# Kernel tuning notes

Measured on AMD Instinct MI355X. Metric: run time of the kernel, lower is better.

## Reference

```python
import jax, jax.numpy as jnp
import numpy as np

TOKENS, D_MODEL, D_FF, RANK = 16384, 1024, 2816, 16


def setup_inputs() -> dict:
    key = jax.random.key(0)
    ks = jax.random.split(key, 7)
    s = lambda k, shp, scale: jax.random.normal(k, shp, dtype=jnp.float32) * scale
    return {
        "x": s(ks[0], (TOKENS, D_MODEL), 1.0),
        "W_gate_up": s(ks[1], (D_MODEL, 2 * D_FF), 0.02),
        "A_gate_up": s(ks[2], (D_MODEL, RANK), 0.02),
        "B_gate_up": s(ks[3], (RANK, 2 * D_FF), 0.02),
        "W_down": s(ks[4], (D_FF, D_MODEL), 0.02),
        "A_down": s(ks[5], (D_FF, RANK), 0.02),
        "B_down": s(ks[6], (RANK, D_MODEL), 0.02),
    }


def reference(x, W_gate_up, A_gate_up, B_gate_up, W_down, A_down, B_down):
    # gate_up_proj: base GEMM + LoRA low-rank correction
    gate_up = x @ W_gate_up + (x @ A_gate_up) @ B_gate_up  # [T, 2*D_FF]
    gate, up = jnp.split(gate_up, 2, axis=-1)
    h = jax.nn.silu(gate) * up  # SiluAndMul, [T, D_FF]
    # down_proj: base GEMM + LoRA correction
    out = h @ W_down + (h @ A_down) @ B_down  # [T, D_MODEL]
    return out
```

## Files before the change

### kernel.cpp

```cpp
#include <hip/hip_runtime.h>


typedef __bf16 bf16_t;
typedef __bf16 bf16x4 __attribute__((ext_vector_type(4)));
typedef __bf16 bf16x8 __attribute__((ext_vector_type(8)));
typedef float f32x4 __attribute__((ext_vector_type(4)));

#define TOKENS 16384
#define DMODEL 1024
#define DFF    2816
#define N2F    5632

#define BARM() asm volatile("s_barrier" ::: "memory")
#define VMW(n) asm volatile("s_waitcnt vmcnt(" #n ")" ::: "memory")
#define MFMA(d, va, vb) d = __builtin_amdgcn_mfma_f32_16x16x32_bf16(va, vb, d, 0, 0, 0)
#define LD8(p) (*(const bf16x8*)(p))
#define SGB(m, n) __builtin_amdgcn_sched_group_barrier(m, n, 0)
#define SGB_PATTERN2() do {                                                       \
    SGB(0x010, 8);                                                                \
    SGB(0x100, 2); SGB(0x008, 5);                                                 \
    SGB(0x100, 2); SGB(0x008, 5);                                                 \
    SGB(0x100, 2); SGB(0x008, 5);                                                 \
    SGB(0x100, 2); SGB(0x008, 5);                                                 \
    SGB(0x100, 2); SGB(0x008, 5);                                                 \
    SGB(0x100, 2); SGB(0x008, 5);                                                 \
    SGB(0x100, 2); SGB(0x008, 5);                                                 \
    SGB(0x100, 2); SGB(0x008, 5);                                                 \
    SGB(0x100, 2); SGB(0x008, 5);                                                 \
    SGB(0x100, 2); SGB(0x008, 5);                                                 \
    SGB(0x100, 2); SGB(0x008, 7);                                                 \
    SGB(0x100, 2); SGB(0x008, 7); } while (0)

__device__ __forceinline__ void gload16(const bf16_t* g, bf16_t* l) {
    __builtin_amdgcn_global_load_lds(
        (const __attribute__((address_space(1))) void*)g,
        (__attribute__((address_space(3))) void*)l, 16, 0, 0);
}

template<int KTOT, int NTOT>
__global__ __launch_bounds__(256) void prep_weff(
        const float* __restrict__ W, const float* __restrict__ A,
        const float* __restrict__ B, bf16_t* __restrict__ Wt) {
    __shared__ float Ws[64][65];
    __shared__ float As[64][17];
    __shared__ float Bs[16][64];
    const int t = threadIdx.x;
    const int k0 = blockIdx.x * 64, n0 = blockIdx.y * 64;
    #pragma unroll
    for (int i = 0; i < 16; ++i) {
        int row = i * 4 + t / 64, col = t % 64;
        Ws[row][col] = W[(size_t)(k0 + row) * NTOT + n0 + col];
    }
    #pragma unroll
    for (int i = 0; i < 4; ++i) {
        int idx = i * 256 + t;
        As[idx / 16][idx % 16] = A[(size_t)(k0 + idx / 16) * 16 + idx % 16];
    }
    #pragma unroll
    for (int i = 0; i < 4; ++i) {
        int idx = i * 256 + t;
        Bs[idx / 64][idx % 64] = B[(size_t)(idx / 64) * NTOT + n0 + idx % 64];
    }
    __syncthreads();
    const int kl = t % 64;
    #pragma unroll
    for (int j = 0; j < 16; ++j) {
        int nl = j * 4 + t / 64;
        float val = Ws[kl][nl];
        #pragma unroll
        for (int r = 0; r < 16; ++r) val += As[kl][r] * Bs[r][nl];
        Wt[(size_t)(n0 + nl) * KTOT + k0 + kl] = (bf16_t)val;
    }
}

__global__ __launch_bounds__(256) void conv_bf16(
        const float* __restrict__ in, bf16_t* __restrict__ out, int n4) {
    int i = blockIdx.x * 256 + threadIdx.x;
    if (i < n4) {
        float4 v = ((const float4*)in)[i];
        bf16x4 o;
        o.x = (bf16_t)v.x; o.y = (bf16_t)v.y; o.z = (bf16_t)v.z; o.w = (bf16_t)v.w;
        ((bf16x4*)out)[i] = o;
    }
}

__global__ __launch_bounds__(512, 2) void gemm1(
        const bf16_t* __restrict__ X, const bf16_t* __restrict__ Wt,
        bf16_t* __restrict__ H) {
    __shared__ bf16_t lds[65536];
    const int t = threadIdx.x, l = t & 63;
    const int wid = t >> 6, wr = wid >> 2, wc = wid & 3;
    const int l15 = l & 15, lhi = l >> 4;
    const int wgl = ((int)blockIdx.x & 7) * 176 + ((int)blockIdx.x >> 3);
    const int tf = wgl % 22, tm = wgl / 22;
    const int mbase = tm * 256, fbase = tf * 128;
    const int srow = t >> 2;
    const int sc8 = ((t & 3) ^ (srow & 3)) * 8;
    const bf16_t* gA  = X + (size_t)(mbase + srow) * DMODEL + sc8;
    const bf16_t* gA2 = gA + (size_t)128 * DMODEL;
    const bf16_t* gBg = Wt + (size_t)(fbase + srow) * DMODEL + sc8;
    const bf16_t* gBu = Wt + (size_t)(DFF + fbase + srow) * DMODEL + sc8;
    const int rsw = (lhi ^ (l15 & 3)) * 8;
    const int aoff = (wr * 128 + l15) * 32 + rsw;
    const int boff = 8192 + (wc * 32 + l15) * 32 + rsw;

    f32x4 accg[8][2] = {}, accu[8][2] = {};
    bf16x8 a0[8], g0[2], u0[2], a1[8], g1[2], u1[2];
    const int NT1 = DMODEL / 32;

#define G1_STAGE(kt) do { const int kc = (kt) * 32;                               \
    bf16_t* p = lds + (((kt) & 3) << 14) + wid * 512;                             \
    gload16(gA  + kc, p);                                                         \
    gload16(gA2 + kc, p + 4096);                                                  \
    gload16(gBg + kc, p + 8192);                                                  \
    gload16(gBu + kc, p + 12288); } while (0)
#define G1_READ(aa, gg, uu, bi) do {                                              \
    const bf16_t* _pa = lds + ((bi) << 14) + aoff;                                \
    aa[0] = LD8(_pa);        aa[1] = LD8(_pa + 512);                              \
    aa[2] = LD8(_pa + 1024); aa[3] = LD8(_pa + 1536);                             \
    aa[4] = LD8(_pa + 2048); aa[5] = LD8(_pa + 2560);                             \
    aa[6] = LD8(_pa + 3072); aa[7] = LD8(_pa + 3584);                             \
    const bf16_t* _pb = lds + ((bi) << 14) + boff;                                \
    gg[0] = LD8(_pb);        gg[1] = LD8(_pb + 512);                              \
    uu[0] = LD8(_pb + 4096); uu[1] = LD8(_pb + 4608); } while (0)
#define G1_MFMA(aa, gg, uu) do {                                                  \
    _Pragma("unroll")                                                             \
    for (int m = 0; m < 8; ++m) {                                                 \
        MFMA(accg[m][0], aa[m], gg[0]); MFMA(accu[m][0], aa[m], uu[0]);           \
        MFMA(accg[m][1], aa[m], gg[1]); MFMA(accu[m][1], aa[m], uu[1]);           \
    } } while (0)

    G1_STAGE(0); G1_STAGE(1);
    VMW(0); BARM();
    G1_STAGE(2); G1_STAGE(3);
    G1_READ(a0, g0, u0, 0);
    G1_READ(a1, g1, u1, 1);
    G1_MFMA(a0, g0, u0);
    for (int s2 = 2; s2 <= NT1 - 2; s2 += 2) {
        VMW(0); BARM();
        if (s2 + 2 < NT1) { G1_STAGE(s2 + 2); G1_STAGE(s2 + 3); }
        G1_READ(a0, g0, u0, s2 & 3);
        G1_MFMA(a1, g1, u1);
        G1_READ(a1, g1, u1, (s2 + 1) & 3);
        G1_MFMA(a0, g0, u0);
        SGB_PATTERN2();
    }
    G1_MFMA(a1, g1, u1);
#undef G1_STAGE
#undef G1_READ
#undef G1_MFMA

    #pragma unroll
    for (int m = 0; m < 8; ++m)
        #pragma unroll
        for (int n = 0; n < 2; ++n)
            #pragma unroll
            for (int r = 0; r < 4; ++r) {
                int row = mbase + wr * 128 + m * 16 + lhi * 4 + r;
                int col = fbase + wc * 32 + n * 16 + l15;
                float g = accg[m][n][r], u = accu[m][n][r];
                H[(size_t)row * DFF + col] = (bf16_t)(g / (1.0f + __expf(-g)) * u);
            }
}

__global__ __launch_bounds__(512, 2) void gemm2(
        const bf16_t* __restrict__ Hm, const bf16_t* __restrict__ Wt,
        float* __restrict__ O) {
    __shared__ bf16_t lds[65536];
    const int t = threadIdx.x, l = t & 63;
    const int wid = t >> 6, wr = wid >> 2, wc = wid & 3;
    const int l15 = l & 15, lhi = l >> 4;
    const int wgl = ((int)blockIdx.x & 7) * 32 + ((int)blockIdx.x >> 3);
    const int tn = wgl % 4, tm = wgl / 4;
    const int mbase = tm * 256, nbase = tn * 256;
    const int srow = t >> 2;
    const int sc8 = ((t & 3) ^ (srow & 3)) * 8;
    const bf16_t* gA  = Hm + (size_t)(mbase + srow) * DFF + sc8;
    const bf16_t* gA2 = gA + (size_t)128 * DFF;
    const bf16_t* gB  = Wt + (size_t)(nbase + srow) * DFF + sc8;
    const bf16_t* gB2 = gB + (size_t)128 * DFF;
    const int rsw = (lhi ^ (l15 & 3)) * 8;
    const int aoff = (wr * 128 + l15) * 32 + rsw;
    const int boff = 8192 + (wc * 64 + l15) * 32 + rsw;

    f32x4 acc[8][4] = {};
    bf16x8 a0[8], b0[4], a1[8], b1[4];
    const int NT2 = DFF / 32;

#define G2_STAGE(kt) do { const int kc = (kt) * 32;                               \
    bf16_t* p = lds + (((kt) & 3) << 14) + wid * 512;                             \
    gload16(gA  + kc, p);                                                         \
    gload16(gA2 + kc, p + 4096);                                                  \
    gload16(gB  + kc, p + 8192);                                                  \
    gload16(gB2 + kc, p + 12288); } while (0)
#define G2_READ(aa, bb, bi) do {                                                  \
    const bf16_t* _pa = lds + ((bi) << 14) + aoff;                                \
    aa[0] = LD8(_pa);        aa[1] = LD8(_pa + 512);                              \
    aa[2] = LD8(_pa + 1024); aa[3] = LD8(_pa + 1536);                             \
    aa[4] = LD8(_pa + 2048); aa[5] = LD8(_pa + 2560);                             \
    aa[6] = LD8(_pa + 3072); aa[7] = LD8(_pa + 3584);                             \
    const bf16_t* _pb = lds + ((bi) << 14) + boff;                                \
    bb[0] = LD8(_pb);        bb[1] = LD8(_pb + 512);                              \
    bb[2] = LD8(_pb + 1024); bb[3] = LD8(_pb + 1536); } while (0)
#define G2_MFMA(aa, bb) do {                                                      \
    _Pragma("unroll")                                                             \
    for (int m = 0; m < 8; ++m) {                                                 \
        MFMA(acc[m][0], aa[m], bb[0]); MFMA(acc[m][1], aa[m], bb[1]);             \
        MFMA(acc[m][2], aa[m], bb[2]); MFMA(acc[m][3], aa[m], bb[3]);             \
    } } while (0)

    G2_STAGE(0); G2_STAGE(1);
    VMW(0); BARM();
    G2_STAGE(2); G2_STAGE(3);
    G2_READ(a0, b0, 0);
    G2_READ(a1, b1, 1);
    G2_MFMA(a0, b0);
    for (int s2 = 2; s2 <= NT2 - 2; s2 += 2) {
        VMW(0); BARM();
        if (s2 + 2 < NT2) { G2_STAGE(s2 + 2); G2_STAGE(s2 + 3); }
        G2_READ(a0, b0, s2 & 3);
        G2_MFMA(a1, b1);
        G2_READ(a1, b1, (s2 + 1) & 3);
        G2_MFMA(a0, b0);
        SGB_PATTERN2();
    }
    G2_MFMA(a1, b1);
#undef G2_STAGE
#undef G2_READ
#undef G2_MFMA

    #pragma unroll
    for (int m = 0; m < 8; ++m)
        #pragma unroll
        for (int n = 0; n < 4; ++n)
            #pragma unroll
            for (int r = 0; r < 4; ++r) {
                int row = mbase + wr * 128 + m * 16 + lhi * 4 + r;
                int col = nbase + wc * 64 + n * 16 + l15;
                O[(size_t)row * DMODEL + col] = acc[m][n][r];
            }
}

extern "C" void kernel_launch(void* const* d_in, const int* in_sizes, int n_in,
                              void* d_out, int out_size, void* d_ws, size_t ws_size,
                              hipStream_t stream) {
    const float* x   = (const float*)d_in[0];
    const float* Wgu = (const float*)d_in[1];
    const float* Agu = (const float*)d_in[2];
    const float* Bgu = (const float*)d_in[3];
    const float* Wd  = (const float*)d_in[4];
    const float* Ad  = (const float*)d_in[5];
    const float* Bd  = (const float*)d_in[6];
    float* out = (float*)d_out;
    char* ws = (char*)d_ws;

    bf16_t* wgut = (bf16_t*)(ws);
    bf16_t* wdt  = (bf16_t*)(ws + 11534336);
    bf16_t* xb   = (bf16_t*)(ws + 17301504);
    bf16_t* hb   = (bf16_t*)(ws + 50855936);

    prep_weff<DMODEL, N2F><<<dim3(DMODEL / 64, N2F / 64), 256, 0, stream>>>(
        Wgu, Agu, Bgu, wgut);
    prep_weff<DFF, DMODEL><<<dim3(DFF / 64, DMODEL / 64), 256, 0, stream>>>(
        Wd, Ad, Bd, wdt);
    conv_bf16<<<(TOKENS * DMODEL / 4) / 256, 256, 0, stream>>>(
        x, xb, TOKENS * DMODEL / 4);
    gemm1<<<22 * 64, 512, 0, stream>>>(xb, wgut, hb);
    gemm2<<<8 * 32, 512, 0, stream>>>(hb, wdt, out);
}
```

Baseline: 327.6 us.

## Restructure gemm1 K-loop into per-tile pipeline with 3-deep prefetch and partial waits

```diff
diff --git a/kernel.cpp b/kernel.cpp
--- a/kernel.cpp
+++ b/kernel.cpp
@@ -16,6 +16,14 @@
 #define MFMA(d, va, vb) d = __builtin_amdgcn_mfma_f32_16x16x32_bf16(va, vb, d, 0, 0, 0)
 #define LD8(p) (*(const bf16x8*)(p))
 #define SGB(m, n) __builtin_amdgcn_sched_group_barrier(m, n, 0)
+#define SGB_PATTERN() do {                                                        \
+    SGB(0x010, 4);                                                                \
+    SGB(0x100, 2); SGB(0x008, 5);                                                 \
+    SGB(0x100, 2); SGB(0x008, 5);                                                 \
+    SGB(0x100, 2); SGB(0x008, 5);                                                 \
+    SGB(0x100, 2); SGB(0x008, 5);                                                 \
+    SGB(0x100, 2); SGB(0x008, 6);                                                 \
+    SGB(0x100, 2); SGB(0x008, 6); } while (0)
 #define SGB_PATTERN2() do {                                                       \
     SGB(0x010, 8);                                                                \
     SGB(0x100, 2); SGB(0x008, 5);                                                 \
@@ -129,23 +137,25 @@
         MFMA(accg[m][0], aa[m], gg[0]); MFMA(accu[m][0], aa[m], uu[0]);           \
         MFMA(accg[m][1], aa[m], gg[1]); MFMA(accu[m][1], aa[m], uu[1]);           \
     } } while (0)
-
-    G1_STAGE(0); G1_STAGE(1);
+#define G1_ITER(kt, aaU, ggU, uuU, aaR, ggR, uuR) do {                            \
+    VMW(4); BARM();                                                               \
+    if ((kt) + 3 < NT1) G1_STAGE((kt) + 3);                                       \
+    G1_READ(aaR, ggR, uuR, ((kt) + 1) & 3);                                       \
+    G1_MFMA(aaU, ggU, uuU);                                                       \
+    SGB_PATTERN(); } while (0)
+
+    G1_STAGE(0); G1_STAGE(1); G1_STAGE(2);
+    VMW(8); BARM();
+    G1_READ(a0, g0, u0, 0);
+    for (int kt2 = 0; kt2 < NT1 - 2; kt2 += 2) {
+        G1_ITER(kt2,     a0, g0, u0, a1, g1, u1);
+        G1_ITER(kt2 + 1, a1, g1, u1, a0, g0, u0);
+    }
     VMW(0); BARM();
-    G1_STAGE(2); G1_STAGE(3);
-    G1_READ(a0, g0, u0, 0);
-    G1_READ(a1, g1, u1, 1);
+    G1_READ(a1, g1, u1, (NT1 - 1) & 3);
     G1_MFMA(a0, g0, u0);
-    for (int s2 = 2; s2 <= NT1 - 2; s2 += 2) {
-        VMW(0); BARM();
-        if (s2 + 2 < NT1) { G1_STAGE(s2 + 2); G1_STAGE(s2 + 3); }
-        G1_READ(a0, g0, u0, s2 & 3);
-        G1_MFMA(a1, g1, u1);
-        G1_READ(a1, g1, u1, (s2 + 1) & 3);
-        G1_MFMA(a0, g0, u0);
-        SGB_PATTERN2();
-    }
     G1_MFMA(a1, g1, u1);
+#undef G1_ITER
 #undef G1_STAGE
 #undef G1_READ
 #undef G1_MFMA
```

New measurement: 329.6 us. Within noise of the previous version (+0.6%).
